# Performance work log

Measured on AMD Instinct MI355X. Metric: run time of the kernel, lower is better.

## Reference

```python
import jax, jax.numpy as jnp
import numpy as np

N_CELLS = 16384
N_SPOTS = 4096
N_LABELS = 512
EXTENT = 1000.0  # spatial extent of the array in microns
UNDERFLOW_NU = 1e-12


def setup_inputs() -> dict:
    key = jax.random.key(0)
    k_z, k_x, k_y, k_lab = jax.random.split(key, 4)
    z = jax.random.uniform(k_z, (N_CELLS, 2), dtype=jnp.float32) * EXTENT
    encoding_x = jax.random.uniform(k_x, (N_SPOTS,), dtype=jnp.float32) * EXTENT
    encoding_y = jax.random.uniform(k_y, (N_SPOTS,), dtype=jnp.float32) * EXTENT
    spot_labels = jax.random.randint(k_lab, (N_SPOTS,), 0, N_LABELS, dtype=jnp.int32)
    diffusion_constant = jnp.float32(2500.0)  # D ~ (50 um)^2 scale so kernel is non-degenerate
    return {
        "z": z,
        "diffusion_constant": diffusion_constant,
        "encoding_x": encoding_x,
        "encoding_y": encoding_y,
        "spot_labels": spot_labels,
    }


def reference(z, diffusion_constant, encoding_x, encoding_y, spot_labels):
    # rel_distances: squared euclidean distance, (n_cells, n_spots)
    dx = encoding_x[None, :] - z[:, 0:1]
    dy = encoding_y[None, :] - z[:, 1:2]
    distances = dx * dx + dy * dy
    # diffusion_kernel (Fick's law, 2D Gaussian kernel)
    norm = 1.0 / (2.0 * jnp.pi * diffusion_constant)
    rate_per_spot = norm * jnp.exp(-distances / (2.0 * diffusion_constant)) + UNDERFLOW_NU
    # label_transfer_rate: segment-sum over spots grouped by label -> (n_cells, n_labels)
    rate_per_tag = jax.ops.segment_sum(
        rate_per_spot.T, spot_labels, num_segments=N_LABELS
    ).T
    return rate_per_tag
```

## Files before the change

### kernel.cpp

```cpp
#include <hip/hip_runtime.h>
#include <hip/hip_bf16.h>

#define N_CELLS  16384
#define N_SPOTS  4096
#define N_LABELS 512
#define NTHREADS 512
#define CPB      8
#define NPAIR    (CPB/2)
#define TABLE    6144

typedef float v2f __attribute__((ext_vector_type(2)));

#if defined(__has_builtin)
#if __has_builtin(__builtin_amdgcn_exp2f)
#define FAST_EXP2(x) __builtin_amdgcn_exp2f(x)
#else
#define FAST_EXP2(x) exp2f(x)
#endif
#else
#define FAST_EXP2(x) exp2f(x)
#endif

#define HALF_LOG2E 0.72134752044448170f

__global__ __launch_bounds__(512) void build_kernel(
    const float* __restrict__ ex, const float* __restrict__ ey,
    const int* __restrict__ labels, const float* __restrict__ dconst,
    float2* __restrict__ table, int* __restrict__ meta)
{
    __shared__ unsigned short s_lab[N_SPOTS];
    __shared__ int s_c[N_LABELS];
    __shared__ int s_h2[128];
    __shared__ int s_suf[128];
    __shared__ int s_pcw[32 * 8];
    __shared__ int s_rlab[N_LABELS];
    __shared__ int s_rcnt[N_LABELS];
    __shared__ int s_wmax[8];
    __shared__ int s_wbase[8];
    __shared__ int s_slot[N_LABELS];
    __shared__ int s_occ[N_LABELS];

    const int t = threadIdx.x;
    const int lane = t & 63, w = t >> 6;

    s_c[t] = 0;
    if (t < 128) s_h2[t] = 0;
    for (int i = t; i < N_SPOTS; i += NTHREADS) s_lab[i] = (unsigned short)labels[i];
    __syncthreads();

    for (int i = t; i < N_SPOTS; i += NTHREADS) atomicAdd(&s_c[s_lab[i]], 1);
    __syncthreads();

    const int myc  = s_c[t];
    const int mycc = myc < 127 ? myc : 127;
    atomicAdd(&s_h2[mycc], 1);
    __syncthreads();

    if (t < 128) s_suf[t] = s_h2[t];
    __syncthreads();
    for (int off = 1; off < 128; off <<= 1) {
        int add = (t < 128 && t + off < 128) ? s_suf[t + off] : 0;
        __syncthreads();
        if (t < 128) s_suf[t] += add;
        __syncthreads();
    }

    int pos_w = 0;
    for (int v = 0; v < 32; ++v) {
        unsigned long long mask = __ballot(myc == v);
        if (myc == v) pos_w = __popcll(mask & ((1ull << lane) - 1ull));
        if (lane == 0) s_pcw[v * 8 + w] = __popcll(mask);
    }
    __syncthreads();
    int pos;
    if (myc < 32) {
        pos = pos_w;
        for (int w2 = 0; w2 < w; ++w2) pos += s_pcw[myc * 8 + w2];
    } else {
        pos = 0;
        for (int j = 0; j < t; ++j) pos += (s_c[j] == myc) ? 1 : 0;
    }
    const int r = ((myc < 127) ? s_suf[myc + 1] : 0) + pos;
    s_rlab[r] = t;
    s_rcnt[r] = myc;
    __syncthreads();

    int v = s_rcnt[t];
    #pragma unroll
    for (int off = 32; off; off >>= 1) { int o = __shfl_xor(v, off); v = v > o ? v : o; }
    if (lane == 0) s_wmax[w] = v;
    __syncthreads();
    if (t == 0) {
        int pb = 0;
        #pragma unroll
        for (int w2 = 0; w2 < 8; ++w2) { s_wbase[w2] = 64 * pb; pb += s_wmax[w2]; }
    }
    __syncthreads();

    const int mytrip = s_wmax[w];
    const int wbase  = s_wbase[w];
    const int mycnt  = s_rcnt[t];

    s_slot[s_rlab[t]] = wbase + lane;
    s_occ[s_rlab[t]]  = 0;
    __syncthreads();

    const float Dv = dconst[0];
    const float sc = sqrtf(HALF_LOG2E / Dv);

    for (int i = t; i < N_SPOTS; i += NTHREADS) {
        int l = s_lab[i];
        int k = atomicAdd(&s_occ[l], 1);
        table[s_slot[l] + k * 64] = make_float2(ex[i] * sc, ey[i] * sc);
    }

    for (int k = mycnt; k < mytrip; ++k)
        table[wbase + k * 64 + lane] = make_float2(1e8f, 0.0f);

    meta[t]                = wbase;
    meta[NTHREADS + t]     = mytrip;
    meta[2 * NTHREADS + t] = s_rlab[t];
    meta[3 * NTHREADS + t] = mycnt;
}

__global__ __launch_bounds__(512) void diffusion_main_kernel(
    const float* __restrict__ z, const float* __restrict__ dconst,
    const v2f* __restrict__ table, const int* __restrict__ meta,
    float* __restrict__ out)
{
    __shared__ float tr[CPB * N_LABELS];

    const int t = threadIdx.x;
    const int lane = t & 63, w = t >> 6;

    const int c = (w + (int)blockIdx.x) & 7;
    const int u = c * 64 + lane;

    const int wbase  = __builtin_amdgcn_readfirstlane(meta[u]);
    const int trip   = __builtin_amdgcn_readfirstlane(meta[NTHREADS + u]);
    const int my_lab = meta[2 * NTHREADS + u];
    const float cntf = (float)meta[3 * NTHREADS + u];

    const float D    = dconst[0];
    const float sc   = sqrtf(HALF_LOG2E / D);
    const float norm = 1.0f / (6.28318530717958647f * D);
    const float base = cntf * 1e-12f;

    const int cell0 = blockIdx.x * CPB;
    v2f zxn[NPAIR], zyn[NPAIR], acc[NPAIR];
    #pragma unroll
    for (int j = 0; j < NPAIR; ++j) {
        zxn[j] = (v2f){ -z[2 * (cell0 + 2 * j)]     * sc,
                        -z[2 * (cell0 + 2 * j + 1)] * sc };
        zyn[j] = (v2f){ -z[2 * (cell0 + 2 * j) + 1]     * sc,
                        -z[2 * (cell0 + 2 * j + 1) + 1] * sc };
        acc[j] = (v2f){0.f, 0.f};
    }

    const v2f* seg = table + wbase + lane;
    if (trip > 0) {
        const int last = trip - 1;
        v2f buf0 = seg[0];
        v2f buf1 = seg[(size_t)(1 < last ? 1 : last) * 64];
        for (int p = 0; p < trip; ++p) {
            const v2f xy = buf0;
            buf0 = buf1;
            const int pn = (p + 2 < last) ? p + 2 : last;
            buf1 = seg[(size_t)pn * 64];
            const v2f xx = (v2f){xy.x, xy.x};
            const v2f yy = (v2f){xy.y, xy.y};
            #pragma unroll
            for (int j = 0; j < NPAIR; ++j) {
                v2f dx  = xx + zxn[j];
                v2f dy  = yy + zyn[j];
                v2f m   = dy * dy;
                v2f nd2 = __builtin_elementwise_fma(-dx, dx, -m);
                v2f e   = (v2f){ FAST_EXP2(nd2.x), FAST_EXP2(nd2.y) };
                acc[j] += e;
            }
        }
    }

    #pragma unroll
    for (int j = 0; j < NPAIR; ++j) {
        tr[(2 * j)     * N_LABELS + my_lab] = fmaf(acc[j].x, norm, base);
        tr[(2 * j + 1) * N_LABELS + my_lab] = fmaf(acc[j].y, norm, base);
    }
    __syncthreads();

    const float4* tr4 = (const float4*)tr;
    float4* out4 = (float4*)(out + (size_t)cell0 * N_LABELS);
    #pragma unroll
    for (int rr = 0; rr < CPB * N_LABELS / 4 / NTHREADS; ++rr)
        out4[t + rr * NTHREADS] = tr4[t + rr * NTHREADS];
}

extern "C" void kernel_launch(void* const* d_in, const int* in_sizes, int n_in,
                              void* d_out, int out_size, void* d_ws, size_t ws_size,
                              hipStream_t stream)
{
    const float* z      = (const float*)d_in[0];
    const float* dconst = (const float*)d_in[1];
    const float* ex     = (const float*)d_in[2];
    const float* ey     = (const float*)d_in[3];
    const int*   labels = (const int*)d_in[4];
    float*       out    = (float*)d_out;

    float2* table = (float2*)d_ws;
    int*    meta  = (int*)((char*)d_ws + (size_t)TABLE * sizeof(float2));

    build_kernel<<<1, NTHREADS, 0, stream>>>(ex, ey, labels, dconst, table, meta);

    diffusion_main_kernel<<<N_CELLS / CPB, NTHREADS, 0, stream>>>(
        z, dconst, (const v2f*)table, meta, out);
}
```

Before: 34.38 us.

## Split table build across eight blocks with per-chunk label histograms

Result: faster. 31.50 us (-8.4%).

```diff
diff --git a/kernel.cpp b/kernel.cpp
--- a/kernel.cpp
+++ b/kernel.cpp
@@ -5,6 +5,7 @@
 #define N_SPOTS  4096
 #define N_LABELS 512
 #define NTHREADS 512
+#define NBUILD   8
 #define CPB      8
 #define NPAIR    (CPB/2)
 #define TABLE    6144
@@ -29,6 +30,7 @@
     float2* __restrict__ table, int* __restrict__ meta)
 {
     __shared__ unsigned short s_lab[N_SPOTS];
+    __shared__ int s_h[NBUILD][N_LABELS];
     __shared__ int s_c[N_LABELS];
     __shared__ int s_h2[128];
     __shared__ int s_suf[128];
@@ -38,20 +40,28 @@
     __shared__ int s_wmax[8];
     __shared__ int s_wbase[8];
     __shared__ int s_slot[N_LABELS];
-    __shared__ int s_occ[N_LABELS];
+    __shared__ int s_kcur[N_LABELS];
 
     const int t = threadIdx.x;
     const int lane = t & 63, w = t >> 6;
-
-    s_c[t] = 0;
+    const int b = blockIdx.x;
+
+    #pragma unroll
+    for (int q = 0; q < NBUILD; ++q) s_h[q][t] = 0;
     if (t < 128) s_h2[t] = 0;
     for (int i = t; i < N_SPOTS; i += NTHREADS) s_lab[i] = (unsigned short)labels[i];
     __syncthreads();
 
-    for (int i = t; i < N_SPOTS; i += NTHREADS) atomicAdd(&s_c[s_lab[i]], 1);
-    __syncthreads();
-
-    const int myc  = s_c[t];
+    for (int i = t; i < N_SPOTS; i += NTHREADS) atomicAdd(&s_h[i >> 9][s_lab[i]], 1);
+    __syncthreads();
+
+    int myc = 0, pre = 0;
+    #pragma unroll
+    for (int q = 0; q < NBUILD; ++q) {
+        if (q == b) pre = myc;
+        myc += s_h[q][t];
+    }
+    s_c[t] = myc;
     const int mycc = myc < 127 ? myc : 127;
     atomicAdd(&s_h2[mycc], 1);
     __syncthreads();
@@ -97,30 +107,34 @@
     }
     __syncthreads();
 
-    const int mytrip = s_wmax[w];
-    const int wbase  = s_wbase[w];
-    const int mycnt  = s_rcnt[t];
-
-    s_slot[s_rlab[t]] = wbase + lane;
-    s_occ[s_rlab[t]]  = 0;
+    s_slot[t] = s_wbase[r >> 6] + (r & 63);
+    s_kcur[t] = pre;
     __syncthreads();
 
     const float Dv = dconst[0];
     const float sc = sqrtf(HALF_LOG2E / Dv);
 
-    for (int i = t; i < N_SPOTS; i += NTHREADS) {
-        int l = s_lab[i];
-        int k = atomicAdd(&s_occ[l], 1);
+    {
+        const int i = b * NTHREADS + t;
+        const int l = s_lab[i];
+        const int k = atomicAdd(&s_kcur[l], 1);
         table[s_slot[l] + k * 64] = make_float2(ex[i] * sc, ey[i] * sc);
     }
 
-    for (int k = mycnt; k < mytrip; ++k)
-        table[wbase + k * 64 + lane] = make_float2(1e8f, 0.0f);
-
-    meta[t]                = wbase;
-    meta[NTHREADS + t]     = mytrip;
-    meta[2 * NTHREADS + t] = s_rlab[t];
-    meta[3 * NTHREADS + t] = mycnt;
+    {
+        const int q    = b * 64 + lane;
+        const int trip = s_wmax[b];
+        const int base = s_wbase[b];
+        for (int k = s_rcnt[q] + (t >> 6); k < trip; k += 8)
+            table[base + k * 64 + lane] = make_float2(1e8f, 0.0f);
+    }
+
+    if (b == 0) {
+        meta[t]                = s_wbase[t >> 6];
+        meta[NTHREADS + t]     = s_wmax[t >> 6];
+        meta[2 * NTHREADS + t] = s_rlab[t];
+        meta[3 * NTHREADS + t] = s_rcnt[t];
+    }
 }
 
 __global__ __launch_bounds__(512) void diffusion_main_kernel(
@@ -209,7 +223,7 @@
     float2* table = (float2*)d_ws;
     int*    meta  = (int*)((char*)d_ws + (size_t)TABLE * sizeof(float2));
 
-    build_kernel<<<1, NTHREADS, 0, stream>>>(ex, ey, labels, dconst, table, meta);
+    build_kernel<<<NBUILD, NTHREADS, 0, stream>>>(ex, ey, labels, dconst, table, meta);
 
     diffusion_main_kernel<<<N_CELLS / CPB, NTHREADS, 0, stream>>>(
         z, dconst, (const v2f*)table, meta, out);
```
